# Optimization experiments

Measured on AMD Instinct MI355X. Metric: run time of the kernel, lower is better.

The kernel has to match this reference:

```python
import jax, jax.numpy as jnp
import numpy as np

D_IN = 4096
NUM_HEADS = 32
HEAD_DIM = 128
NUM_KV = 8
GROUP = NUM_HEADS // NUM_KV
EPS = 1e-6
ROPE_BASE = 10000.0


def rms_norm(x, scale):
    # norm over last dim (head_dim), computed in fp32 as in torch ref
    var = jnp.mean(x * x, axis=-1, keepdims=True)
    return x * jax.lax.rsqrt(var + EPS) * scale


def rope_cos_sin(positions, dim):
    inv_freq = 1.0 / (ROPE_BASE ** (jnp.arange(0, dim, 2, dtype=jnp.float32) / dim))
    angles = positions.astype(jnp.float32)[:, None] * inv_freq[None, :]  # (N, dim/2)
    angles = jnp.concatenate([angles, angles], axis=-1)  # (N, dim)
    return jnp.cos(angles), jnp.sin(angles)


def apply_rope(t, cos, sin):
    # t: (N, heads, D); cos/sin: (N, D)
    half = t.shape[-1] // 2
    rot = jnp.concatenate([-t[..., half:], t[..., :half]], axis=-1)
    return t * cos[:, None, :] + rot * sin[:, None, :]


def setup_inputs() -> dict:
    key = jax.random.key(0)
    ks = jax.random.split(key, 6)
    B, S = 1, 2048
    x = jax.random.normal(ks[0], (B, S, D_IN), dtype=jnp.float32)
    positions = jnp.arange(B * S, dtype=jnp.int32)
    sc = 0.02
    Wq = jax.random.normal(ks[1], (D_IN, NUM_HEADS * HEAD_DIM), dtype=jnp.float32) * sc
    Wk = jax.random.normal(ks[2], (D_IN, NUM_KV * HEAD_DIM), dtype=jnp.float32) * sc
    Wv = jax.random.normal(ks[3], (D_IN, NUM_KV * HEAD_DIM), dtype=jnp.float32) * sc
    Wo = jax.random.normal(ks[4], (NUM_HEADS * HEAD_DIM, D_IN), dtype=jnp.float32) * sc
    q_scale = jnp.ones((HEAD_DIM,), dtype=jnp.float32)
    k_scale = jnp.ones((HEAD_DIM,), dtype=jnp.float32)
    return {"x": x, "positions": positions, "Wq": Wq, "Wk": Wk, "Wv": Wv,
            "Wo": Wo, "q_scale": q_scale, "k_scale": k_scale}


def reference(x, positions, Wq, Wk, Wv, Wo, q_scale, k_scale):
    B, S, _ = x.shape
    N = B * S
    xf = x.reshape(N, D_IN)
    q = (xf @ Wq).reshape(N, NUM_HEADS, HEAD_DIM)
    k = (xf @ Wk).reshape(N, NUM_KV, HEAD_DIM)
    v = (xf @ Wv).reshape(N, NUM_KV, HEAD_DIM)
    # QK RMSNorm over head_dim
    q = rms_norm(q, q_scale)
    k = rms_norm(k, k_scale)
    # RoPE (rotate-half)
    cos, sin = rope_cos_sin(positions, HEAD_DIM)
    q = apply_rope(q, cos, sin)
    k = apply_rope(k, cos, sin)
    # (B, KV, group, S, D) for q; (B, KV, S, D) for k, v  (GQA broadcast)
    q = q.reshape(B, S, NUM_KV, GROUP, HEAD_DIM).transpose(0, 2, 3, 1, 4)
    k = k.reshape(B, S, NUM_KV, HEAD_DIM).transpose(0, 2, 1, 3)
    v = v.reshape(B, S, NUM_KV, HEAD_DIM).transpose(0, 2, 1, 3)
    scale = 1.0 / jnp.sqrt(jnp.float32(HEAD_DIM))
    scores = jnp.einsum('bghsd,bgtd->bghst', q, k) * scale  # (B,KV,G,S,S)
    causal = jnp.tril(jnp.ones((S, S), dtype=bool))
    scores = jnp.where(causal[None, None, None, :, :], scores, jnp.finfo(scores.dtype).min)
    attn = jax.nn.softmax(scores, axis=-1)
    ctx = jnp.einsum('bghst,bgtd->bghsd', attn, v)  # (B,KV,G,S,D)
    ctx = ctx.transpose(0, 3, 1, 2, 4).reshape(B, S, NUM_HEADS * HEAD_DIM)
    return ctx @ Wo
```

## Files before the change

kernel.cpp:

```cpp
#include <hip/hip_runtime.h>

#define S_LEN 2048
#define DMODEL 4096
#define NQKV 6144

typedef unsigned short u16;
typedef __attribute__((ext_vector_type(8))) short bf16x8;
typedef __attribute__((ext_vector_type(8))) unsigned short u16x8;
typedef __attribute__((ext_vector_type(4))) float f32x4;

#define NEG_BIG (-3.0e38f)

__device__ __forceinline__ float bf2f(u16 h) {
    union { unsigned u; float f; } c; c.u = ((unsigned)h) << 16; return c.f;
}
__device__ __forceinline__ u16 f2bf(float x) {
    union { float f; unsigned u; } c; c.f = x;
    return (u16)((c.u + 0x7fffu + ((c.u >> 16) & 1u)) >> 16);
}

__device__ __forceinline__ void gload16(const void* g, void* l) {
    __builtin_amdgcn_global_load_lds(
        (const __attribute__((address_space(1))) void*)g,
        (__attribute__((address_space(3))) void*)l, 16, 0, 0);
}

__global__ __launch_bounds__(256) void detect_dtype(const u16* __restrict__ probe,
                                                    int* __restrict__ flags) {
    __shared__ int bad_s;
    if (threadIdx.x == 0) bad_s = 0;
    __syncthreads();
    int bad = 0;
    for (int i = threadIdx.x; i < 16384; i += 256) {
        float v = bf2f(probe[i]);
        if (!(fabsf(v) < 1e6f)) bad = 1;
    }
    if (bad) atomicOr(&bad_s, 1);
    __syncthreads();
    if (threadIdx.x == 0) { flags[0] = bad_s; flags[1] = 0; }
}

__global__ __launch_bounds__(256) void conv_bf16(const void* __restrict__ src,
                                                 u16* __restrict__ dst, long n,
                                                 const int* __restrict__ flag) {
    const bool f32 = (*flag != 0);
    long i = (long)blockIdx.x * 256 + threadIdx.x;
    long stride = (long)gridDim.x * 256;
    for (; i < n; i += stride) {
        float v = f32 ? ((const float*)src)[i] : bf2f(((const u16*)src)[i]);
        dst[i] = f2bf(v);
    }
}

__global__ __launch_bounds__(256) void transpose_any(
        const void* __restrict__ src, long base_off, long sld, long szoff,
        u16* __restrict__ dst, long dld, long dzoff,
        const int* __restrict__ flag) {
    __shared__ alignas(16) u16 tile[32][33];
    const bool f32 = (*flag != 0);
    u16* d = dst + (long)blockIdx.z * dzoff;
    long soff = base_off + (long)blockIdx.z * szoff;
    int c0 = blockIdx.x * 32, r0 = blockIdx.y * 32;
    int tx = threadIdx.x & 31, ty = threadIdx.x >> 5;
    for (int i = 0; i < 32; i += 8) {
        long idx = soff + (long)(r0 + ty + i) * sld + c0 + tx;
        float v = f32 ? ((const float*)src)[idx] : bf2f(((const u16*)src)[idx]);
        tile[ty + i][tx] = f2bf(v);
    }
    __syncthreads();
    for (int i = 0; i < 32; i += 8)
        d[(long)(c0 + ty + i) * dld + r0 + tx] = tile[tx][ty + i];
}

__global__ __launch_bounds__(256, 2) void gemm_bt(
        const u16* __restrict__ A, const u16* __restrict__ BT,
        u16* __restrict__ C, int K, int ldc) {
    __shared__ alignas(16) u16 Asm[128 * 64];
    __shared__ alignas(16) u16 Bsm[128 * 64];
    const int tid = threadIdx.x;
    const int lane = tid & 63, wid = tid >> 6;
    const int wm = wid >> 1, wn = wid & 1;
    const int lm = lane & 15, lq = lane >> 4;
    const int m0 = blockIdx.y * 128, n0 = blockIdx.x * 128;

    f32x4 acc[4][4] = {};
    const int nk = K >> 6;
    for (int kt = 0; kt < nk; ++kt) {
        const int k0 = kt << 6;
        __syncthreads();
        for (int i = 0; i < 4; ++i) {
            int g = i * 256 + tid;
            int r = g >> 3, kg = g & 7;
            gload16(A  + (size_t)(m0 + r) * K + k0 + kg * 8,
                    Asm + (size_t)(i * 256 + wid * 64) * 8);
            gload16(BT + (size_t)(n0 + r) * K + k0 + kg * 8,
                    Bsm + (size_t)(i * 256 + wid * 64) * 8);
        }
        __syncthreads();
        for (int ks = 0; ks < 2; ++ks) {
            bf16x8 af[4], bfr[4];
            for (int i = 0; i < 4; ++i)
                af[i] = *(const bf16x8*)(const void*)(Asm + (wm * 64 + i * 16 + lm) * 64 + ks * 32 + lq * 8);
            for (int i = 0; i < 4; ++i)
                bfr[i] = *(const bf16x8*)(const void*)(Bsm + (wn * 64 + i * 16 + lm) * 64 + ks * 32 + lq * 8);
            for (int mi = 0; mi < 4; ++mi)
                for (int ni = 0; ni < 4; ++ni)
                    acc[mi][ni] = __builtin_amdgcn_mfma_f32_16x16x32_bf16(af[mi], bfr[ni], acc[mi][ni], 0, 0, 0);
        }
    }
    for (int mi = 0; mi < 4; ++mi)
        for (int ni = 0; ni < 4; ++ni) {
            int col = n0 + wn * 64 + ni * 16 + lm;
            int rowb = m0 + wm * 64 + mi * 16 + lq * 4;
            for (int r = 0; r < 4; ++r)
                C[(size_t)(rowb + r) * ldc + col] = f2bf(acc[mi][ni][r]);
        }
}

__global__ __launch_bounds__(256, 2) void gemm_bt_f32(
        const u16* __restrict__ A, const u16* __restrict__ BT,
        float* __restrict__ C, int K, int ldc) {
    __shared__ alignas(16) u16 Asm[128 * 64];
    __shared__ alignas(16) u16 Bsm[128 * 64];
    const int tid = threadIdx.x;
    const int lane = tid & 63, wid = tid >> 6;
    const int wm = wid >> 1, wn = wid & 1;
    const int lm = lane & 15, lq = lane >> 4;
    const int m0 = blockIdx.y * 128, n0 = blockIdx.x * 128;

    f32x4 acc[4][4] = {};
    const int nk = K >> 6;
    for (int kt = 0; kt < nk; ++kt) {
        const int k0 = kt << 6;
        __syncthreads();
        for (int i = 0; i < 4; ++i) {
            int g = i * 256 + tid;
            int r = g >> 3, kg = g & 7;
            gload16(A  + (size_t)(m0 + r) * K + k0 + kg * 8,
                    Asm + (size_t)(i * 256 + wid * 64) * 8);
            gload16(BT + (size_t)(n0 + r) * K + k0 + kg * 8,
                    Bsm + (size_t)(i * 256 + wid * 64) * 8);
        }
        __syncthreads();
        for (int ks = 0; ks < 2; ++ks) {
            bf16x8 af[4], bfr[4];
            for (int i = 0; i < 4; ++i)
                af[i] = *(const bf16x8*)(const void*)(Asm + (wm * 64 + i * 16 + lm) * 64 + ks * 32 + lq * 8);
            for (int i = 0; i < 4; ++i)
                bfr[i] = *(const bf16x8*)(const void*)(Bsm + (wn * 64 + i * 16 + lm) * 64 + ks * 32 + lq * 8);
            for (int mi = 0; mi < 4; ++mi)
                for (int ni = 0; ni < 4; ++ni)
                    acc[mi][ni] = __builtin_amdgcn_mfma_f32_16x16x32_bf16(af[mi], bfr[ni], acc[mi][ni], 0, 0, 0);
        }
    }
    for (int mi = 0; mi < 4; ++mi)
        for (int ni = 0; ni < 4; ++ni) {
            int col = n0 + wn * 64 + ni * 16 + lm;
            int rowb = m0 + wm * 64 + mi * 16 + lq * 4;
            for (int r = 0; r < 4; ++r)
                C[(size_t)(rowb + r) * ldc + col] = acc[mi][ni][r];
        }
}

__global__ __launch_bounds__(256) void rms_rope(
        const u16* __restrict__ qkv, const int* __restrict__ pos,
        const u16* __restrict__ qs, const u16* __restrict__ kscale,
        u16* __restrict__ Qb, u16* __restrict__ Kb) {
    int w = threadIdx.x >> 6, lane = threadIdx.x & 63;
    int task = blockIdx.x * 4 + w;
    int h = task >> 11, row = task & 2047;
    int base = (h < 32) ? h * 128 : 4096 + (h - 32) * 128;
    const u16* src = qkv + (size_t)row * NQKV + base;
    float t0 = bf2f(src[lane]), t1 = bf2f(src[lane + 64]);
    float ss = t0 * t0 + t1 * t1;
    for (int m = 1; m < 64; m <<= 1) ss += __shfl_xor(ss, m);
    float inv = rsqrtf(ss * (1.0f / 128.0f) + 1e-6f);
    const u16* sc = (h < 32) ? qs : kscale;
    float n0 = t0 * inv * bf2f(sc[lane]);
    float n1 = t1 * inv * bf2f(sc[lane + 64]);
    float p = (float)pos[row];
    float ang = p * __expf(-(float)lane * (9.210340371976184f / 64.0f));
    float c = cosf(ang), s = sinf(ang);
    float o0 = n0 * c - n1 * s;
    float o1 = n1 * c + n0 * s;
    float mul = (h < 32) ? 0.08838834764831845f : 1.0f;
    u16* dst = (h < 32) ? (Qb + ((size_t)h * S_LEN + row) * 128)
                        : (Kb + ((size_t)(h - 32) * S_LEN + row) * 128);
    dst[lane] = f2bf(o0 * mul);
    dst[lane + 64] = f2bf(o1 * mul);
}

__global__ __launch_bounds__(256, 2) void flash_attn(
        const u16* __restrict__ Qb, const u16* __restrict__ Kb,
        const u16* __restrict__ VTb, u16* __restrict__ ctx) {
    const int h = blockIdx.y, kvh = h >> 2;
    const int tid = threadIdx.x, lane = tid & 63, w = tid >> 6;
    const int lm = lane & 15, lq = lane >> 4;
    const int swz = (lm & 7) << 3;
    __shared__ alignas(16) u16 smem[20480];
    u16* Ksm = smem;
    u16* Vsm = smem + 8192;
    u16* Psm = smem + 16384;
    const u16* Kh = Kb + (size_t)kvh * S_LEN * 128;
    const u16* Vh = VTb + (size_t)kvh * 128 * S_LEN;

    for (int pass = 0; pass < 2; ++pass) {
        const int t = pass ? (31 - blockIdx.x) : blockIdx.x;
        const u16* Qh = Qb + ((size_t)h * S_LEN + (size_t)t * 64) * 128;

        __syncthreads();
        for (int i = 0; i < 4; ++i) {
            int g = i * 256 + tid;
            int row = g >> 4, s = g & 15;
            int sp = (s & 8) | ((s ^ row) & 7);
            gload16(Qh + (size_t)row * 128 + sp * 8,
                    Ksm + (size_t)(i * 256 + w * 64) * 8);
        }
        __syncthreads();
        bf16x8 aq[4];
        for (int ks = 0; ks < 4; ++ks)
            aq[ks] = *(const bf16x8*)(const void*)(
                Ksm + (((w * 16 + lm) * 128 + ks * 32 + lq * 8) ^ swz));

        float mrow[4], lrow[4];
        f32x4 accO[8];
        const f32x4 zero = {0.f, 0.f, 0.f, 0.f};
        for (int r = 0; r < 4; ++r) { mrow[r] = NEG_BIG; lrow[r] = 0.f; }
        for (int di = 0; di < 8; ++di) accO[di] = zero;

        for (int j = 0; j <= t; ++j) {
            __syncthreads();
            for (int i = 0; i < 4; ++i) {
                int g = i * 256 + tid;
                int row = g >> 4, s = g & 15;
                int sp = (s & 8) | ((s ^ row) & 7);
                gload16(Kh + (size_t)(j * 64 + row) * 128 + sp * 8,
                        Ksm + (size_t)(i * 256 + w * 64) * 8);
            }
            for (int i = 0; i < 4; ++i) {
                int g = i * 256 + tid;
                int d = g >> 3, s = g & 7;
                int sp = s ^ (d & 7);
                gload16(Vh + (size_t)d * S_LEN + j * 64 + sp * 8,
                        Vsm + (size_t)(i * 256 + w * 64) * 8);
            }
            __syncthreads();

            f32x4 sacc[4] = {};
            for (int ks = 0; ks < 4; ++ks) {
                bf16x8 kf[4];
                for (int ni = 0; ni < 4; ++ni)
                    kf[ni] = *(const bf16x8*)(const void*)(
                        Ksm + (((ni * 16 + lm) * 128 + ks * 32 + lq * 8) ^ swz));
                for (int ni = 0; ni < 4; ++ni)
                    sacc[ni] = __builtin_amdgcn_mfma_f32_16x16x32_bf16(aq[ks], kf[ni], sacc[ni], 0, 0, 0);
            }

            if (j == t) {
                for (int ni = 0; ni < 4; ++ni) {
                    int col = ni * 16 + lm;
                    for (int r = 0; r < 4; ++r)
                        if (col > w * 16 + lq * 4 + r) sacc[ni][r] = NEG_BIG;
                }
            }

            for (int r = 0; r < 4; ++r) {
                float mx = fmaxf(fmaxf(sacc[0][r], sacc[1][r]),
                                 fmaxf(sacc[2][r], sacc[3][r]));
                for (int sft = 1; sft < 16; sft <<= 1) mx = fmaxf(mx, __shfl_xor(mx, sft));
                float mN = fmaxf(mrow[r], mx);
                float alpha = __expf(mrow[r] - mN);
                mrow[r] = mN;
                float psum = 0.f;
                int prow = w * 16 + lq * 4 + r;
                for (int ni = 0; ni < 4; ++ni) {
                    float pv = __expf(sacc[ni][r] - mN);
                    psum += pv;
                    Psm[prow * 64 + ((ni * 16 + lm) ^ ((prow & 7) << 3))] = f2bf(pv);
                }
                for (int sft = 1; sft < 16; sft <<= 1) psum += __shfl_xor(psum, sft);
                lrow[r] = lrow[r] * alpha + psum;
                for (int di = 0; di < 8; ++di) accO[di][r] *= alpha;
            }
            __syncthreads();

            for (int ks2 = 0; ks2 < 2; ++ks2) {
                bf16x8 pf = *(const bf16x8*)(const void*)(
                    Psm + (((w * 16 + lm) * 64 + ks2 * 32 + lq * 8) ^ swz));
                for (int di = 0; di < 8; ++di) {
                    bf16x8 vf = *(const bf16x8*)(const void*)(
                        Vsm + (((di * 16 + lm) * 64 + ks2 * 32 + lq * 8) ^ swz));
                    accO[di] = __builtin_amdgcn_mfma_f32_16x16x32_bf16(pf, vf, accO[di], 0, 0, 0);
                }
            }
        }

        for (int r = 0; r < 4; ++r) {
            float invl = 1.0f / fmaxf(lrow[r], 1e-30f);
            size_t rowg = (size_t)t * 64 + w * 16 + lq * 4 + r;
            for (int di = 0; di < 8; ++di)
                ctx[rowg * 4096 + h * 128 + di * 16 + lm] = f2bf(accO[di][r] * invl);
        }
    }
}

extern "C" void kernel_launch(void* const* d_in, const int* in_sizes, int n_in,
                              void* d_out, int out_size, void* d_ws, size_t ws_size,
                              hipStream_t stream) {
    const void* x   = d_in[0];
    const int* pos  = (const int*)d_in[1];
    const void* Wq  = d_in[2];
    const void* Wk  = d_in[3];
    const void* Wv  = d_in[4];
    const void* Wo  = d_in[5];
    const void* qs  = d_in[6];
    const void* ks  = d_in[7];

    if (ws_size < (size_t)145 * 1024 * 1024) return;
    char* ws = (char*)d_ws;
    u16* WqkvT = (u16*)ws;
    u16* WoT   = (u16*)(ws + (size_t)48  * 1024 * 1024);
    u16* qkv   = (u16*)(ws + (size_t)80  * 1024 * 1024);
    u16* ctx   = qkv;
    u16* Qb    = (u16*)(ws + (size_t)104 * 1024 * 1024);
    u16* Kb    = (u16*)(ws + (size_t)120 * 1024 * 1024);
    u16* VTb   = (u16*)(ws + (size_t)124 * 1024 * 1024);
    u16* xb    = (u16*)(ws + (size_t)128 * 1024 * 1024);
    int* flags = (int*)(ws + (size_t)144 * 1024 * 1024);
    u16* qsb   = (u16*)(ws + (size_t)144 * 1024 * 1024 + 1024);
    u16* ksb   = (u16*)(ws + (size_t)144 * 1024 * 1024 + 2048);

    dim3 b256(256);
    const int* flag  = flags;
    const int* fzero = flags + 1;

    detect_dtype<<<1, b256, 0, stream>>>((const u16*)Wq, flags);
    conv_bf16<<<8192, b256, 0, stream>>>(x,  xb,  (long)S_LEN * DMODEL, flag);
    conv_bf16<<<1,    b256, 0, stream>>>(qs, qsb, 128, flag);
    conv_bf16<<<1,    b256, 0, stream>>>(ks, ksb, 128, flag);

    transpose_any<<<dim3(128, 128, 1), b256, 0, stream>>>(Wq, 0, 4096, 0, WqkvT, 4096, 0, flag);
    transpose_any<<<dim3(32, 128, 1),  b256, 0, stream>>>(Wk, 0, 1024, 0, WqkvT + (size_t)4096 * 4096, 4096, 0, flag);
    transpose_any<<<dim3(32, 128, 1),  b256, 0, stream>>>(Wv, 0, 1024, 0, WqkvT + (size_t)5120 * 4096, 4096, 0, flag);
    transpose_any<<<dim3(128, 128, 1), b256, 0, stream>>>(Wo, 0, 4096, 0, WoT, 4096, 0, flag);

    gemm_bt<<<dim3(48, 16), b256, 0, stream>>>(xb, WqkvT, qkv, 4096, NQKV);
    rms_rope<<<dim3(20480), b256, 0, stream>>>(qkv, pos, qsb, ksb, Qb, Kb);
    transpose_any<<<dim3(4, 64, 8), b256, 0, stream>>>(qkv, 5120, NQKV, 128, VTb, 2048, (long)128 * 2048, fzero);
    flash_attn<<<dim3(16, 32), b256, 0, stream>>>(Qb, Kb, VTb, ctx);
    gemm_bt_f32<<<dim3(32, 16), b256, 0, stream>>>(ctx, WoT, (float*)d_out, 4096, 4096);
}
```

Measured before the change: 580.8 us.

## Replace GEMMs with 4-stage pipelined, LDS-swizzled 256x128 tile kernel

Both projection GEMMs (QKV and output) now share one templated core. It uses 512-thread blocks computing 256x128 tiles with K-steps of 32. A 4-buffer LDS ring keeps three global-to-LDS stages in flight, tracked with explicit vmcnt waits, and replaces the old load-then-compute loop that synchronized twice per step. LDS chunks are XOR-swizzled to reduce bank conflicts, and MFMA issue is raised with setprio. The risks are the larger LDS footprint and lower occupancy of one block per CU, plus a 1.5-wave tail on the QKV grid of 384 blocks.

Measured after the change: 573.0 us. About the same (-1.3%).

```diff
diff --git a/kernel.cpp b/kernel.cpp
--- a/kernel.cpp
+++ b/kernel.cpp
@@ -23,6 +23,12 @@
     __builtin_amdgcn_global_load_lds(
         (const __attribute__((address_space(1))) void*)g,
         (__attribute__((address_space(3))) void*)l, 16, 0, 0);
+}
+
+__device__ __forceinline__ void barfence() {
+    asm volatile("" ::: "memory");
+    __builtin_amdgcn_s_barrier();
+    asm volatile("" ::: "memory");
 }
 
 __global__ __launch_bounds__(256) void detect_dtype(const u16* __restrict__ probe,
@@ -72,94 +78,99 @@
         d[(long)(c0 + ty + i) * dld + r0 + tx] = tile[tx][ty + i];
 }
 
-__global__ __launch_bounds__(256, 2) void gemm_bt(
+__device__ __forceinline__ void st_out(u16* C, size_t idx, float v)   { C[idx] = f2bf(v); }
+__device__ __forceinline__ void st_out(float* C, size_t idx, float v) { C[idx] = v; }
+
+template <typename OUT>
+__device__ __forceinline__ void gemm_dp_core(
+        const u16* __restrict__ A, const u16* __restrict__ BT,
+        OUT* __restrict__ C, int K, int ldc) {
+    __shared__ alignas(16) u16 smem[4 * 12288];
+    const int tid = threadIdx.x;
+    const int lane = tid & 63, wid = tid >> 6;
+    const int wr = wid >> 1, wc = wid & 1;
+    const int lm = lane & 15, lq = lane >> 4;
+    const int m0 = blockIdx.y * 256, n0 = blockIdx.x * 128;
+
+    const int cA0 = wid * 64 + lane;
+    const int cA1 = 512 + cA0;
+    const int cB  = wid * 64 + lane;
+    const int rA0 = cA0 >> 2, rA1 = cA1 >> 2, rB = cB >> 2;
+    const int spA0 = ((cA0 & 3) ^ ((rA0 >> 1) & 3)) * 8;
+    const int spA1 = ((cA1 & 3) ^ ((rA1 >> 1) & 3)) * 8;
+    const int spB  = ((cB  & 3) ^ ((rB  >> 1) & 3)) * 8;
+    const u16* aS0 = A  + (size_t)(m0 + rA0) * K + spA0;
+    const u16* aS1 = A  + (size_t)(m0 + rA1) * K + spA1;
+    const u16* bS  = BT + (size_t)(n0 + rB ) * K + spB;
+    const int ldsA0 = (wid * 64) * 8;
+    const int ldsA1 = (512 + wid * 64) * 8;
+    const int ldsB  = 8192 + (wid * 64) * 8;
+
+    const int NK = K >> 5;
+    for (int pt = 0; pt < 3; ++pt) {
+        u16* buf = smem + pt * 12288;
+        const int ko = pt << 5;
+        gload16(aS0 + ko, buf + ldsA0);
+        gload16(aS1 + ko, buf + ldsA1);
+        gload16(bS  + ko, buf + ldsB);
+    }
+    asm volatile("s_waitcnt vmcnt(6)" ::: "memory");
+    barfence();
+
+    f32x4 acc[4][4] = {};
+    const int arow = wr * 64 + lm;
+    const int brow = wc * 64 + lm;
+
+#pragma unroll 4
+    for (int kt = 0; kt < NK; ++kt) {
+        const u16* Ab = smem + (kt & 3) * 12288;
+        const u16* Bb = Ab + 8192;
+        bf16x8 bfv[4], afv[4];
+        for (int ni = 0; ni < 4; ++ni) {
+            int row = brow + ni * 16;
+            bfv[ni] = *(const bf16x8*)(const void*)(Bb + row * 32 + ((lq ^ ((row >> 1) & 3)) << 3));
+        }
+        for (int mi = 0; mi < 4; ++mi) {
+            int row = arow + mi * 16;
+            afv[mi] = *(const bf16x8*)(const void*)(Ab + row * 32 + ((lq ^ ((row >> 1) & 3)) << 3));
+        }
+        if (kt + 3 < NK) {
+            u16* nb = smem + ((kt + 3) & 3) * 12288;
+            const int ko = (kt + 3) << 5;
+            gload16(aS0 + ko, nb + ldsA0);
+            gload16(aS1 + ko, nb + ldsA1);
+            gload16(bS  + ko, nb + ldsB);
+        }
+        barfence();
+        __builtin_amdgcn_s_setprio(1);
+        for (int mi = 0; mi < 4; ++mi)
+            for (int ni = 0; ni < 4; ++ni)
+                acc[mi][ni] = __builtin_amdgcn_mfma_f32_16x16x32_bf16(afv[mi], bfv[ni], acc[mi][ni], 0, 0, 0);
+        __builtin_amdgcn_s_setprio(0);
+        if (kt + 3 < NK)       { asm volatile("s_waitcnt vmcnt(6)" ::: "memory"); }
+        else if (kt + 2 < NK)  { asm volatile("s_waitcnt vmcnt(3)" ::: "memory"); }
+        else if (kt + 1 < NK)  { asm volatile("s_waitcnt vmcnt(0)" ::: "memory"); }
+        barfence();
+    }
+
+    for (int mi = 0; mi < 4; ++mi)
+        for (int ni = 0; ni < 4; ++ni) {
+            int col  = n0 + wc * 64 + ni * 16 + lm;
+            int rowb = m0 + wr * 64 + mi * 16 + lq * 4;
+            for (int r = 0; r < 4; ++r)
+                st_out(C, (size_t)(rowb + r) * ldc + col, acc[mi][ni][r]);
+        }
+}
+
+__global__ __launch_bounds__(512, 1) void gemm_dp_bf16(
         const u16* __restrict__ A, const u16* __restrict__ BT,
         u16* __restrict__ C, int K, int ldc) {
-    __shared__ alignas(16) u16 Asm[128 * 64];
-    __shared__ alignas(16) u16 Bsm[128 * 64];
-    const int tid = threadIdx.x;
-    const int lane = tid & 63, wid = tid >> 6;
-    const int wm = wid >> 1, wn = wid & 1;
-    const int lm = lane & 15, lq = lane >> 4;
-    const int m0 = blockIdx.y * 128, n0 = blockIdx.x * 128;
-
-    f32x4 acc[4][4] = {};
-    const int nk = K >> 6;
-    for (int kt = 0; kt < nk; ++kt) {
-        const int k0 = kt << 6;
-        __syncthreads();
-        for (int i = 0; i < 4; ++i) {
-            int g = i * 256 + tid;
-            int r = g >> 3, kg = g & 7;
-            gload16(A  + (size_t)(m0 + r) * K + k0 + kg * 8,
-                    Asm + (size_t)(i * 256 + wid * 64) * 8);
-            gload16(BT + (size_t)(n0 + r) * K + k0 + kg * 8,
-                    Bsm + (size_t)(i * 256 + wid * 64) * 8);
-        }
-        __syncthreads();
-        for (int ks = 0; ks < 2; ++ks) {
-            bf16x8 af[4], bfr[4];
-            for (int i = 0; i < 4; ++i)
-                af[i] = *(const bf16x8*)(const void*)(Asm + (wm * 64 + i * 16 + lm) * 64 + ks * 32 + lq * 8);
-            for (int i = 0; i < 4; ++i)
-                bfr[i] = *(const bf16x8*)(const void*)(Bsm + (wn * 64 + i * 16 + lm) * 64 + ks * 32 + lq * 8);
-            for (int mi = 0; mi < 4; ++mi)
-                for (int ni = 0; ni < 4; ++ni)
-                    acc[mi][ni] = __builtin_amdgcn_mfma_f32_16x16x32_bf16(af[mi], bfr[ni], acc[mi][ni], 0, 0, 0);
-        }
-    }
-    for (int mi = 0; mi < 4; ++mi)
-        for (int ni = 0; ni < 4; ++ni) {
-            int col = n0 + wn * 64 + ni * 16 + lm;
-            int rowb = m0 + wm * 64 + mi * 16 + lq * 4;
-            for (int r = 0; r < 4; ++r)
-                C[(size_t)(rowb + r) * ldc + col] = f2bf(acc[mi][ni][r]);
-        }
-}
-
-__global__ __launch_bounds__(256, 2) void gemm_bt_f32(
+    gemm_dp_core<u16>(A, BT, C, K, ldc);
+}
+__global__ __launch_bounds__(512, 1) void gemm_dp_f32(
         const u16* __restrict__ A, const u16* __restrict__ BT,
         float* __restrict__ C, int K, int ldc) {
-    __shared__ alignas(16) u16 Asm[128 * 64];
-    __shared__ alignas(16) u16 Bsm[128 * 64];
-    const int tid = threadIdx.x;
-    const int lane = tid & 63, wid = tid >> 6;
-    const int wm = wid >> 1, wn = wid & 1;
-    const int lm = lane & 15, lq = lane >> 4;
-    const int m0 = blockIdx.y * 128, n0 = blockIdx.x * 128;
-
-    f32x4 acc[4][4] = {};
-    const int nk = K >> 6;
-    for (int kt = 0; kt < nk; ++kt) {
-        const int k0 = kt << 6;
-        __syncthreads();
-        for (int i = 0; i < 4; ++i) {
-            int g = i * 256 + tid;
-            int r = g >> 3, kg = g & 7;
-            gload16(A  + (size_t)(m0 + r) * K + k0 + kg * 8,
-                    Asm + (size_t)(i * 256 + wid * 64) * 8);
-            gload16(BT + (size_t)(n0 + r) * K + k0 + kg * 8,
-                    Bsm + (size_t)(i * 256 + wid * 64) * 8);
-        }
-        __syncthreads();
-        for (int ks = 0; ks < 2; ++ks) {
-            bf16x8 af[4], bfr[4];
-            for (int i = 0; i < 4; ++i)
-                af[i] = *(const bf16x8*)(const void*)(Asm + (wm * 64 + i * 16 + lm) * 64 + ks * 32 + lq * 8);
-            for (int i = 0; i < 4; ++i)
-                bfr[i] = *(const bf16x8*)(const void*)(Bsm + (wn * 64 + i * 16 + lm) * 64 + ks * 32 + lq * 8);
-            for (int mi = 0; mi < 4; ++mi)
-                for (int ni = 0; ni < 4; ++ni)
-                    acc[mi][ni] = __builtin_amdgcn_mfma_f32_16x16x32_bf16(af[mi], bfr[ni], acc[mi][ni], 0, 0, 0);
-        }
-    }
-    for (int mi = 0; mi < 4; ++mi)
-        for (int ni = 0; ni < 4; ++ni) {
-            int col = n0 + wn * 64 + ni * 16 + lm;
-            int rowb = m0 + wm * 64 + mi * 16 + lq * 4;
-            for (int r = 0; r < 4; ++r)
-                C[(size_t)(rowb + r) * ldc + col] = acc[mi][ni][r];
-        }
+    gemm_dp_core<float>(A, BT, C, K, ldc);
 }
 
 __global__ __launch_bounds__(256) void rms_rope(
@@ -344,9 +355,9 @@
     transpose_any<<<dim3(32, 128, 1),  b256, 0, stream>>>(Wv, 0, 1024, 0, WqkvT + (size_t)5120 * 4096, 4096, 0, flag);
     transpose_any<<<dim3(128, 128, 1), b256, 0, stream>>>(Wo, 0, 4096, 0, WoT, 4096, 0, flag);
 
-    gemm_bt<<<dim3(48, 16), b256, 0, stream>>>(xb, WqkvT, qkv, 4096, NQKV);
+    gemm_dp_bf16<<<dim3(48, 8), dim3(512), 0, stream>>>(xb, WqkvT, qkv, 4096, NQKV);
     rms_rope<<<dim3(20480), b256, 0, stream>>>(qkv, pos, qsb, ksb, Qb, Kb);
     transpose_any<<<dim3(4, 64, 8), b256, 0, stream>>>(qkv, 5120, NQKV, 128, VTb, 2048, (long)128 * 2048, fzero);
     flash_attn<<<dim3(16, 32), b256, 0, stream>>>(Qb, Kb, VTb, ctx);
-    gemm_bt_f32<<<dim3(32, 16), b256, 0, stream>>>(ctx, WoT, (float*)d_out, 4096, 4096);
-}
+    gemm_dp_f32<<<dim3(32, 8), dim3(512), 0, stream>>>(ctx, WoT, (float*)d_out, 4096, 4096);
+}
```
